# Kernel tuning notes

Measured on AMD Instinct MI355X. Metric: run time of the kernel, lower is better.

The kernel has to match this reference:

```python
import jax, jax.numpy as jnp
import numpy as np

DIM = 512
HEADS = 8
DIM_HEAD = 64
INNER = HEADS * DIM_HEAD          # 512
CPB_DIM = DIM // 2                # 256 (ContinuousPositionBias hidden dim)
FF_INNER = int(DIM * 4 * 2 / 3)   # 1365 (GEGLU inner dim)
B, C, F, H, W = 2, 512, 8, 32, 32
SCALE = DIM_HEAD ** -0.5


def setup_inputs() -> dict:
    key = jax.random.key(0)
    ks = jax.random.split(key, 24)
    def rnd(k, shape, s=0.02):
        return jax.random.normal(k, shape, jnp.float32) * s
    return {
        "x": jax.random.normal(ks[0], (B, C, F, W, W), jnp.float32)[:, :, :, :H, :],
        # spatial attention
        "sa_gamma": jnp.ones((DIM,), jnp.float32),
        "sa_wq": rnd(ks[1], (DIM, INNER)),
        "sa_wkv": rnd(ks[2], (DIM, 2 * INNER)),
        "sa_wo": rnd(ks[3], (INNER, DIM)),
        # temporal attention
        "ta_gamma": jnp.ones((DIM,), jnp.float32),
        "ta_wq": rnd(ks[4], (DIM, INNER)),
        "ta_wkv": rnd(ks[5], (DIM, 2 * INNER)),
        "ta_wo": rnd(ks[6], (INNER, DIM)),
        # spatial ContinuousPositionBias MLP (num_dims=2, layers=2)
        "sp_w1": rnd(ks[7], (2, CPB_DIM), 0.1), "sp_b1": jnp.zeros((CPB_DIM,), jnp.float32),
        "sp_w2": rnd(ks[8], (CPB_DIM, CPB_DIM), 0.05), "sp_b2": jnp.zeros((CPB_DIM,), jnp.float32),
        "sp_w3": rnd(ks[9], (CPB_DIM, HEADS), 0.05), "sp_b3": jnp.zeros((HEADS,), jnp.float32),
        # temporal ContinuousPositionBias MLP (num_dims=1)
        "tp_w1": rnd(ks[10], (1, CPB_DIM), 0.1), "tp_b1": jnp.zeros((CPB_DIM,), jnp.float32),
        "tp_w2": rnd(ks[11], (CPB_DIM, CPB_DIM), 0.05), "tp_b2": jnp.zeros((CPB_DIM,), jnp.float32),
        "tp_w3": rnd(ks[12], (CPB_DIM, HEADS), 0.05), "tp_b3": jnp.zeros((HEADS,), jnp.float32),
        # FeedForward: Conv3d 1x1 (no bias) -> GEGLU -> RMSNorm -> Conv3d 1x1
        "ff_win": rnd(ks[13], (DIM, 2 * FF_INNER)),
        "ff_gamma": jnp.ones((FF_INNER,), jnp.float32),
        "ff_wout": rnd(ks[14], (FF_INNER, DIM)),
    }


def _rms_last(x, g):
    # torch: F.normalize(x, dim=-1) * sqrt(C) * gamma
    nrm = jnp.sqrt(jnp.sum(x * x, axis=-1, keepdims=True))
    return x / jnp.maximum(nrm, 1e-12) * jnp.sqrt(jnp.float32(x.shape[-1])) * g


def _mlp_bias(rel, w1, b1, w2, b2, w3, b3):
    h = jax.nn.silu(rel @ w1 + b1)
    h = jax.nn.silu(h @ w2 + b2)
    return h @ w3 + b3  # [R, heads]


def _cpb_2d(h, w, params):
    ry = jnp.arange(-(h - 1), h, dtype=jnp.float32)
    rx = jnp.arange(-(w - 1), w, dtype=jnp.float32)
    gy, gx = jnp.meshgrid(ry, rx, indexing='ij')
    rel = jnp.stack([gy, gx], -1).reshape(-1, 2)          # [(2h-1)(2w-1), 2]
    tab = _mlp_bias(rel, *params)                          # [R, heads]
    py, px = jnp.meshgrid(jnp.arange(h), jnp.arange(w), indexing='ij')
    pos = jnp.stack([py.reshape(-1), px.reshape(-1)], -1)  # [n, 2]
    d = pos[:, None, :] - pos[None, :, :]                  # [n, n, 2]
    idx = (d[..., 0] + h - 1) * (2 * w - 1) + (d[..., 1] + w - 1)
    return jnp.transpose(tab[idx], (2, 0, 1))              # [heads, n, n]


def _cpb_1d(f, params):
    rel = jnp.arange(-(f - 1), f, dtype=jnp.float32)[:, None]
    tab = _mlp_bias(rel, *params)                          # [2f-1, heads]
    p = jnp.arange(f)
    idx = p[:, None] - p[None, :] + f - 1
    return jnp.transpose(tab[idx], (2, 0, 1))              # [heads, f, f]


def _attn(x, gamma, wq, wkv, wo, bias):
    # x: [b, n, c]; manual softmax(QK^T*scale + bias)V (flash disabled by pos_bias)
    xn = _rms_last(x, gamma)
    q = xn @ wq
    k, v = jnp.split(xn @ wkv, 2, axis=-1)
    b, n, _ = q.shape
    rs = lambda t: t.reshape(b, n, HEADS, DIM_HEAD).transpose(0, 2, 1, 3)
    q, k, v = rs(q), rs(k), rs(v)
    s = jnp.einsum('bhid,bhjd->bhij', q, k) * SCALE + bias[None]
    a = jax.nn.softmax(s, axis=-1)
    o = jnp.einsum('bhij,bhjd->bhid', a, v)
    o = o.transpose(0, 2, 1, 3).reshape(b, n, INNER)
    return o @ wo


def _ff(x, win, gamma, wout):
    # x: [b, f, h, w, c] channel-last; Conv3d 1x1 == channel einsum
    hdn = jnp.einsum('bfhwc,co->bfhwo', x, win)
    a, gate = jnp.split(hdn, 2, axis=-1)
    y = a * jax.nn.gelu(gate, approximate=False)           # GEGLU (torch exact gelu)
    # shift_token: chunk channels, shift second half by +1 frame
    c1 = (FF_INNER + 1) // 2
    t1, t2 = y[..., :c1], y[..., c1:]
    t2 = jnp.pad(t2, ((0, 0), (1, 0), (0, 0), (0, 0), (0, 0)))[:, :-1]
    y = jnp.concatenate([t1, t2], axis=-1)
    yn = _rms_last(y, gamma)                               # RMSNorm over channels
    return jnp.einsum('bfhwi,ic->bfhwc', yn, wout)


def reference(x, sa_gamma, sa_wq, sa_wkv, sa_wo, ta_gamma, ta_wq, ta_wkv, ta_wo,
              sp_w1, sp_b1, sp_w2, sp_b2, sp_w3, sp_b3,
              tp_w1, tp_b1, tp_w2, tp_b2, tp_w3, tp_b3,
              ff_win, ff_gamma, ff_wout):
    b, c, f, h, w = x.shape
    xl = jnp.transpose(x, (0, 2, 3, 4, 1))                 # b f h w c
    # spatial attention over (h w) tokens, batched over (b f)
    xs = xl.reshape(b * f, h * w, c)
    sp_bias = _cpb_2d(h, w, (sp_w1, sp_b1, sp_w2, sp_b2, sp_w3, sp_b3))
    xs = _attn(xs, sa_gamma, sa_wq, sa_wkv, sa_wo, sp_bias) + xs
    xv = xs.reshape(b, f, h, w, c)
    # temporal attention over f tokens, batched over (b h w)
    xt = jnp.transpose(xv, (0, 2, 3, 1, 4)).reshape(b * h * w, f, c)
    tp_bias = _cpb_1d(f, (tp_w1, tp_b1, tp_w2, tp_b2, tp_w3, tp_b3))
    xt = _attn(xt, ta_gamma, ta_wq, ta_wkv, ta_wo, tp_bias) + xt
    xv = jnp.transpose(xt.reshape(b, h, w, f, c), (0, 3, 1, 2, 4))
    # GEGLU feedforward with token shift
    xv = _ff(xv, ff_win, ff_gamma, ff_wout) + xv
    return jnp.transpose(xv, (0, 4, 1, 2, 3))              # b c f h w
```

## Files before the change

kernel.cpp:

```cpp
#include <hip/hip_runtime.h>
#include <cstdint>
#include <cstddef>

typedef __bf16 bf16_t;
typedef __bf16 bf16x8 __attribute__((ext_vector_type(8)));
typedef float floatx4 __attribute__((ext_vector_type(4)));

__device__ __forceinline__ float wred_sum(float v) {
#pragma unroll
  for (int off = 32; off > 0; off >>= 1) v += __shfl_xor(v, off);
  return v;
}
__device__ __forceinline__ void async16(const void* g, void* l) {
  __builtin_amdgcn_global_load_lds((const __attribute__((address_space(1))) void*)g,
                                   (__attribute__((address_space(3))) void*)l, 16, 0, 0);
}

template <bool OUT_BF16, bool RESID>
__global__ __launch_bounds__(256) void st_gemm(
    const bf16_t* __restrict__ A, const bf16_t* __restrict__ B, void* Cp,
    const float* Res, int M, int N, int K, int lda, int ldb, int ldc, int nb1,
    long long sa1, long long sa2, long long sb1, long long sb2,
    long long sc1, long long sc2) {
  __shared__ bf16_t sA[128 * 32];
  __shared__ bf16_t sB[128 * 32];
  const int z = blockIdx.z;
  const int z1 = z % nb1, z2 = z / nb1;
  A += z1 * sa1 + z2 * sa2;
  B += z1 * sb1 + z2 * sb2;
  const long long coff = z1 * sc1 + z2 * sc2;
  const int tid = threadIdx.x;
  const int bm = blockIdx.x, bn = blockIdx.y;
  const int lane = tid & 63;
  const int wave = tid >> 6;
  const int wm = (wave >> 1) * 64, wn = (wave & 1) * 64;
  const int rowf = lane & 15, kq = (lane >> 4) * 8;

  floatx4 acc[4][4];
#pragma unroll
  for (int i = 0; i < 4; ++i)
#pragma unroll
    for (int j = 0; j < 4; ++j) acc[i][j] = floatx4{0.f, 0.f, 0.f, 0.f};

  for (int kt = 0; kt < K; kt += 32) {
#pragma unroll
    for (int it = 0; it < 2; ++it) {
      int slot = it * 256 + tid;
      int mi = slot >> 2, kc = slot & 3;
      int ar = bm * 128 + mi; if (ar > M - 1) ar = M - 1;
      int br = bn * 128 + mi; if (br > N - 1) br = N - 1;
      async16(A + (size_t)ar * lda + kt + kc * 8, (char*)sA + slot * 16);
      async16(B + (size_t)br * ldb + kt + kc * 8, (char*)sB + slot * 16);
    }
    __syncthreads();
    bf16x8 af[4], bv[4];
#pragma unroll
    for (int i = 0; i < 4; ++i) {
      af[i] = *(const bf16x8*)(sA + (wm + i * 16 + rowf) * 32 + kq);
      bv[i] = *(const bf16x8*)(sB + (wn + i * 16 + rowf) * 32 + kq);
    }
#pragma unroll
    for (int i = 0; i < 4; ++i)
#pragma unroll
      for (int j = 0; j < 4; ++j)
        acc[i][j] = __builtin_amdgcn_mfma_f32_16x16x32_bf16(af[i], bv[j], acc[i][j], 0, 0, 0);
    __syncthreads();
  }

  const int colBase = bn * 128 + wn + (lane & 15);
  const int rowBase = bm * 128 + wm + (lane >> 4) * 4;
#pragma unroll
  for (int i = 0; i < 4; ++i) {
#pragma unroll
    for (int j = 0; j < 4; ++j) {
      int col = colBase + j * 16;
      if (col >= N) continue;
#pragma unroll
      for (int r = 0; r < 4; ++r) {
        int row = rowBase + i * 16 + r;
        if (row >= M) continue;
        long long idx = coff + (long long)row * ldc + col;
        float v = acc[i][j][r];
        if (RESID) v += Res[idx];
        if (OUT_BF16) ((bf16_t*)Cp)[idx] = (bf16_t)v;
        else          ((float*)Cp)[idx] = v;
      }
    }
  }
}

__global__ __launch_bounds__(256) void st_transpose2d(
    const float* __restrict__ in, float* __restrict__ out, int R, int Cc,
    long long inb, long long outb) {
  __shared__ float tile[32][33];
  const int ct = blockIdx.x, rt = blockIdx.y, b = blockIdx.z;
  in += (long long)b * inb;
  out += (long long)b * outb;
  const int tx = threadIdx.x & 31, ty = threadIdx.x >> 5;
#pragma unroll
  for (int k = 0; k < 4; ++k) {
    int r = rt * 32 + ty + k * 8;
    int c = ct * 32 + tx;
    tile[ty + k * 8][tx] = in[(size_t)r * Cc + c];
  }
  __syncthreads();
#pragma unroll
  for (int k = 0; k < 4; ++k) {
    int c = ct * 32 + ty + k * 8;
    int r = rt * 32 + tx;
    out[(size_t)c * R + r] = tile[tx][ty + k * 8];
  }
}

__global__ void st_wtrans(const float* __restrict__ src, bf16_t* __restrict__ dst,
                          int K, int Kpad, int N, int srcld, int coloff, long total) {
  long idx = (long)blockIdx.x * 256 + threadIdx.x;
  if (idx >= total) return;
  int kp = (int)(idx % Kpad);
  int n = (int)(idx / Kpad);
  float v = (kp < K) ? src[(size_t)kp * srcld + coloff + n] : 0.f;
  dst[idx] = (bf16_t)v;
}

__global__ __launch_bounds__(256) void st_cpb(
    const float* __restrict__ w1, const float* __restrict__ b1,
    const float* __restrict__ w2, const float* __restrict__ b2,
    const float* __restrict__ w3, const float* __restrict__ b3,
    bf16_t* __restrict__ tab2d, float* __restrict__ tab1d, int two_d) {
  const int pos = blockIdx.x, t = threadIdx.x;
  float r0, r1 = 0.f;
  if (two_d) { r0 = (float)(pos / 63 - 31); r1 = (float)(pos % 63 - 31); }
  else { r0 = (float)(pos - 7); }
  __shared__ float sh[256];
  float h = r0 * w1[t] + (two_d ? r1 * w1[256 + t] : 0.f) + b1[t];
  h = h / (1.f + expf(-h));
  sh[t] = h;
  __syncthreads();
  float h2 = b2[t];
  for (int j = 0; j < 256; ++j) h2 += sh[j] * w2[j * 256 + t];
  h2 = h2 / (1.f + expf(-h2));
  __syncthreads();
  sh[t] = h2;
  __syncthreads();
  if (t < 8) {
    float o = b3[t];
    for (int j = 0; j < 256; ++j) o += sh[j] * w3[j * 8 + t];
    if (two_d) tab2d[t * 4000 + pos] = (bf16_t)o;
    else tab1d[t * 15 + pos] = o;
  }
}

__global__ __launch_bounds__(256) void st_rmsnorm(const float* __restrict__ x,
                                                  const float* __restrict__ gamma,
                                                  bf16_t* __restrict__ y) {
  const int token = blockIdx.x * 4 + (threadIdx.x >> 6);
  const int lane = threadIdx.x & 63;
  const float* xr = x + (size_t)token * 512;
  float v[8];
  float ss = 0.f;
#pragma unroll
  for (int k = 0; k < 8; ++k) { v[k] = xr[k * 64 + lane]; ss += v[k] * v[k]; }
  ss = wred_sum(ss);
  const float r = 22.627416998f / fmaxf(sqrtf(ss), 1e-12f);
  bf16_t* yr = y + (size_t)token * 512;
#pragma unroll
  for (int k = 0; k < 8; ++k) yr[k * 64 + lane] = (bf16_t)(v[k] * r * gamma[k * 64 + lane]);
}

__global__ __launch_bounds__(256) void st_vtrans(const bf16_t* __restrict__ qkv,
                                                 bf16_t* __restrict__ vT) {
  __shared__ float tile[32][33];
  const int jt = blockIdx.x, dt = blockIdx.y, z = blockIdx.z;
  const int bf = z >> 3, h = z & 7;
  const int tx = threadIdx.x & 31, ty = threadIdx.x >> 5;
#pragma unroll
  for (int k = 0; k < 4; ++k) {
    int j = jt * 32 + ty + k * 8;
    int d = dt * 32 + tx;
    tile[ty + k * 8][tx] = (float)qkv[((size_t)(bf * 1024 + j)) * 1536 + 1024 + h * 64 + d];
  }
  __syncthreads();
#pragma unroll
  for (int k = 0; k < 4; ++k) {
    int d = dt * 32 + ty + k * 8;
    int j = jt * 32 + tx;
    vT[((size_t)z * 64 + d) * 1024 + j] = (bf16_t)tile[tx][ty + k * 8];
  }
}

__global__ __launch_bounds__(256, 3) void st_flash(
    const bf16_t* __restrict__ qkv, const bf16_t* __restrict__ vT,
    const bf16_t* __restrict__ tabb, bf16_t* __restrict__ ob) {
  __shared__ __align__(16) bf16_t ldsK[2][64 * 64];
  __shared__ __align__(16) bf16_t ldsV[2][64 * 64];
  __shared__ __align__(16) bf16_t ldsP[4 * 32 * 64];
  __shared__ __align__(16) bf16_t ldsT[2216];
  const int qtile = blockIdx.x;
  const int z = blockIdx.y;
  const int bf = z >> 3, h = z & 7;
  const int tid = threadIdx.x;
  const int lane = tid & 63, wave = tid >> 6;
  const int cl = lane & 15, g = lane >> 4;
  const size_t qkvBase = (size_t)bf * 1024 * 1536 + h * 64;
  const int eoff = (qtile * 252) & ~7;
  const bf16_t* Kp = qkv + qkvBase + 512;
  const bf16_t* Vp = vT + (size_t)z * 65536;

#pragma unroll
  for (int it = 0; it < 4; ++it) {
    int s = it * 256 + tid;
    int row = s >> 3, c = s & 7;
    int cs = c ^ (row & 7);
    async16(qkv + qkvBase + (size_t)(qtile * 128 + row) * 1536 + cs * 8,
            (char*)ldsP + s * 16);
  }
#pragma unroll
  for (int it = 0; it < 2; ++it) {
    int s = it * 256 + tid;
    if (s < 277) async16(tabb + h * 4000 + eoff + s * 8, (char*)ldsT + s * 16);
  }
#pragma unroll
  for (int it = 0; it < 2; ++it) {
    int s = it * 256 + tid;
    int row = s >> 3, c = s & 7;
    int cs = c ^ (row & 7);
    async16(Kp + (size_t)row * 1536 + cs * 8, (char*)ldsK[0] + s * 16);
    async16(Vp + (size_t)row * 1024 + cs * 8, (char*)ldsV[0] + s * 16);
  }
  __syncthreads();
  bf16x8 aq[2][2];
#pragma unroll
  for (int it = 0; it < 2; ++it)
#pragma unroll
    for (int ks = 0; ks < 2; ++ks) {
      int row = wave * 32 + it * 16 + cl;
      int cs = (g + ks * 4) ^ (row & 7);
      aq[it][ks] = *(const bf16x8*)(ldsP + row * 64 + cs * 8);
    }
  __syncthreads();

  int fiB[2][4];
#pragma unroll
  for (int it = 0; it < 2; ++it)
#pragma unroll
    for (int r = 0; r < 4; ++r) {
      int i = qtile * 128 + wave * 32 + it * 16 + g * 4 + r;
      fiB[it][r] = (i >> 5) * 63 + (i & 31) + 1984 - eoff;
    }
  float lsum[2][4];
  floatx4 oacc[2][4];
#pragma unroll
  for (int it = 0; it < 2; ++it)
#pragma unroll
    for (int r = 0; r < 4; ++r) lsum[it][r] = 0.f;
#pragma unroll
  for (int it = 0; it < 2; ++it)
#pragma unroll
    for (int dt = 0; dt < 4; ++dt) oacc[it][dt] = floatx4{0.f, 0.f, 0.f, 0.f};

  bf16_t* ldsPw = ldsP + wave * (32 * 64);

#pragma unroll 2
  for (int t = 0; t < 16; ++t) {
    const int p = t & 1;
    if (t < 15) {
      const int j1 = (t + 1) * 64;
#pragma unroll
      for (int it = 0; it < 2; ++it) {
        int s = it * 256 + tid;
        int row = s >> 3, c = s & 7;
        int cs = c ^ (row & 7);
        async16(Kp + (size_t)(j1 + row) * 1536 + cs * 8, (char*)ldsK[p ^ 1] + s * 16);
        async16(Vp + (size_t)row * 1024 + j1 + cs * 8, (char*)ldsV[p ^ 1] + s * 16);
      }
    }
    const int j0 = t * 64;
    floatx4 sacc[2][4];
#pragma unroll
    for (int it = 0; it < 2; ++it)
#pragma unroll
      for (int jt = 0; jt < 4; ++jt) sacc[it][jt] = floatx4{0.f, 0.f, 0.f, 0.f};
#pragma unroll
    for (int ks = 0; ks < 2; ++ks) {
#pragma unroll
      for (int jt = 0; jt < 4; ++jt) {
        int col = jt * 16 + cl;
        bf16x8 bk = *(const bf16x8*)(ldsK[p] + col * 64 + ((g + ks * 4) ^ (col & 7)) * 8);
#pragma unroll
        for (int it = 0; it < 2; ++it)
          sacc[it][jt] = __builtin_amdgcn_mfma_f32_16x16x32_bf16(aq[it][ks], bk, sacc[it][jt], 0, 0, 0);
      }
    }
#pragma unroll
    for (int jt = 0; jt < 4; ++jt) {
      int j = j0 + jt * 16 + cl;
      int fj = (j >> 5) * 63 + (j & 31);
      int pg = (jt * 2 + (cl >> 3));
#pragma unroll
      for (int it = 0; it < 2; ++it) {
#pragma unroll
        for (int r = 0; r < 4; ++r) {
          float e = __expf(sacc[it][jt][r] * 0.125f + (float)ldsT[fiB[it][r] - fj]);
          lsum[it][r] += e;
          int prow = it * 16 + g * 4 + r;
          ldsPw[prow * 64 + (pg ^ (prow & 7)) * 8 + (cl & 7)] = (bf16_t)e;
        }
      }
    }
#pragma unroll
    for (int ks = 0; ks < 2; ++ks) {
      bf16x8 ap[2];
#pragma unroll
      for (int it = 0; it < 2; ++it)
        ap[it] = *(const bf16x8*)(ldsPw + (it * 16 + cl) * 64 + ((g + ks * 4) ^ (cl & 7)) * 8);
#pragma unroll
      for (int dt = 0; dt < 4; ++dt) {
        int d = dt * 16 + cl;
        bf16x8 bv = *(const bf16x8*)(ldsV[p] + d * 64 + ((g + ks * 4) ^ (d & 7)) * 8);
#pragma unroll
        for (int it = 0; it < 2; ++it)
          oacc[it][dt] = __builtin_amdgcn_mfma_f32_16x16x32_bf16(ap[it], bv, oacc[it][dt], 0, 0, 0);
      }
    }
    __syncthreads();
  }
#pragma unroll
  for (int it = 0; it < 2; ++it)
#pragma unroll
    for (int r = 0; r < 4; ++r) {
#pragma unroll
      for (int x = 1; x < 16; x <<= 1) lsum[it][r] += __shfl_xor(lsum[it][r], x);
      lsum[it][r] = 1.f / lsum[it][r];
    }
#pragma unroll
  for (int it = 0; it < 2; ++it) {
#pragma unroll
    for (int r = 0; r < 4; ++r) {
      int i = qtile * 128 + wave * 32 + it * 16 + g * 4 + r;
      size_t base = ((size_t)bf * 1024 + i) * 512 + h * 64;
#pragma unroll
      for (int dt = 0; dt < 4; ++dt)
        ob[base + dt * 16 + cl] = (bf16_t)(oacc[it][dt][r] * lsum[it][r]);
    }
  }
}

__global__ __launch_bounds__(256) void st_tattn2(const bf16_t* __restrict__ qkv,
                                                 const float* __restrict__ tabf,
                                                 bf16_t* __restrict__ o) {
  const int wg = blockIdx.x * 4 + (threadIdx.x >> 6);
  const int bhw = wg >> 3, head = wg & 7;
  const int lane = threadIdx.x & 63;
  const size_t base = (size_t)bhw * 8 * 1536 + head * 64 + lane;
  float q[8], k[8], v[8];
#pragma unroll
  for (int f = 0; f < 8; ++f) {
    q[f] = (float)qkv[base + (size_t)f * 1536];
    k[f] = (float)qkv[base + (size_t)f * 1536 + 512];
    v[f] = (float)qkv[base + (size_t)f * 1536 + 1024];
  }
  float p[64];
#pragma unroll
  for (int i = 0; i < 8; ++i)
#pragma unroll
    for (int j = 0; j < 8; ++j) p[i * 8 + j] = q[i] * k[j];
#pragma unroll
  for (int st = 32; st >= 1; st >>= 1) {
    const bool hi = (lane & st) != 0;
#pragma unroll
    for (int m = 0; m < st; ++m) {
      float give = hi ? p[m] : p[m + st];
      float keep = hi ? p[m + st] : p[m];
      p[m] = keep + __shfl_xor(give, st);
    }
  }
  const int i = lane >> 3, j = lane & 7;
  float e = __expf(p[0] * 0.125f + tabf[head * 15 + i - j + 7]);
  float sm = e;
  sm += __shfl_xor(sm, 1);
  sm += __shfl_xor(sm, 2);
  sm += __shfl_xor(sm, 4);
  const float prob = e / sm;
  float acc[8];
#pragma unroll
  for (int ii = 0; ii < 8; ++ii) acc[ii] = 0.f;
#pragma unroll
  for (int ii = 0; ii < 8; ++ii)
#pragma unroll
    for (int jj = 0; jj < 8; ++jj)
      acc[ii] += __shfl(prob, ii * 8 + jj) * v[jj];
#pragma unroll
  for (int ii = 0; ii < 8; ++ii)
    o[(size_t)(bhw * 8 + ii) * 512 + head * 64 + lane] = (bf16_t)acc[ii];
}

__global__ void st_permute(const float* __restrict__ in, float* __restrict__ out, int dir,
                           bf16_t* __restrict__ out2) {
  size_t idx = (size_t)blockIdx.x * 256 + threadIdx.x;
  int c = (int)(idx & 511);
  size_t r = idx >> 9;
  size_t src;
  if (dir == 0) {
    int f = (int)(r & 7);
    int hw = (int)((r >> 3) & 1023);
    int b = (int)(r >> 13);
    src = ((((size_t)b * 8 + f) * 1024 + hw) << 9) + c;
  } else {
    int hw = (int)(r & 1023);
    int f = (int)((r >> 10) & 7);
    int b = (int)(r >> 13);
    src = ((((size_t)b * 1024 + hw) * 8 + f) << 9) + c;
  }
  float v = in[src];
  out[idx] = v;
  if (out2) out2[idx] = (bf16_t)v;
}

__global__ __launch_bounds__(256) void st_glu(const bf16_t* __restrict__ hdn,
                                              const float* __restrict__ gamma,
                                              bf16_t* __restrict__ yn) {
  const int t = blockIdx.x;
  const int tid = threadIdx.x;
  const int f = (t >> 10) & 7;
  float y[6];
  float ss = 0.f;
#pragma unroll
  for (int kk = 0; kk < 6; ++kk) {
    int c = kk * 256 + tid;
    float yv = 0.f;
    if (c < 1365) {
      long src = t;
      bool valid = true;
      if (c >= 683) { if (f == 0) valid = false; else src = t - 1024; }
      if (valid) {
        float av = (float)hdn[src * 2730 + c];
        float gv = (float)hdn[src * 2730 + 1365 + c];
        yv = av * 0.5f * gv * (1.f + erff(gv * 0.70710678f));
      }
    }
    y[kk] = yv;
    ss += yv * yv;
  }
  __shared__ float red[4];
  ss = wred_sum(ss);
  if ((tid & 63) == 0) red[tid >> 6] = ss;
  __syncthreads();
  ss = red[0] + red[1] + red[2] + red[3];
  const float r = sqrtf(1365.f) / fmaxf(sqrtf(ss), 1e-12f);
#pragma unroll
  for (int kk = 0; kk < 6; ++kk) {
    int c = kk * 256 + tid;
    if (c < 1365) yn[(size_t)t * 1376 + c] = (bf16_t)(y[kk] * r * gamma[c]);
  }
  if (tid < 11) yn[(size_t)t * 1376 + 1365 + tid] = (bf16_t)0.f;
}

extern "C" void kernel_launch(void* const* d_in, const int* in_sizes, int n_in,
                              void* d_out, int out_size, void* d_ws, size_t ws_size,
                              hipStream_t stream) {
  const float* x        = (const float*)d_in[0];
  const float* sa_gamma = (const float*)d_in[1];
  const float* sa_wq    = (const float*)d_in[2];
  const float* sa_wkv   = (const float*)d_in[3];
  const float* sa_wo    = (const float*)d_in[4];
  const float* ta_gamma = (const float*)d_in[5];
  const float* ta_wq    = (const float*)d_in[6];
  const float* ta_wkv   = (const float*)d_in[7];
  const float* ta_wo    = (const float*)d_in[8];
  const float* sp_w1 = (const float*)d_in[9];
  const float* sp_b1 = (const float*)d_in[10];
  const float* sp_w2 = (const float*)d_in[11];
  const float* sp_b2 = (const float*)d_in[12];
  const float* sp_w3 = (const float*)d_in[13];
  const float* sp_b3 = (const float*)d_in[14];
  const float* tp_w1 = (const float*)d_in[15];
  const float* tp_b1 = (const float*)d_in[16];
  const float* tp_w2 = (const float*)d_in[17];
  const float* tp_b2 = (const float*)d_in[18];
  const float* tp_w3 = (const float*)d_in[19];
  const float* tp_b3 = (const float*)d_in[20];
  const float* ff_win   = (const float*)d_in[21];
  const float* ff_gamma = (const float*)d_in[22];
  const float* ff_wout  = (const float*)d_in[23];
  float* outp = (float*)d_out;

  char* ws = (char*)d_ws;
  size_t off = 0;
  auto alloc = [&](size_t bytes) -> char* {
    char* p = ws + off;
    off += (bytes + 255) & ~(size_t)255;
    return p;
  };
  const long T = 16384;
  float*  xs  = (float*)alloc((size_t)T * 512 * 4);
  bf16_t* xn  = (bf16_t*)alloc((size_t)T * 512 * 2);
  char*   R2  = alloc((size_t)T * 1536 * 2);
  char*   R3  = alloc((size_t)T * 1536 * 2);
  bf16_t* ynb = (bf16_t*)alloc((size_t)T * 1376 * 2);
  bf16_t* wqkvT_sa = (bf16_t*)alloc(1536ULL * 512 * 2);
  bf16_t* woT_sa   = (bf16_t*)alloc(512ULL * 512 * 2);
  bf16_t* wqkvT_ta = (bf16_t*)alloc(1536ULL * 512 * 2);
  bf16_t* woT_ta   = (bf16_t*)alloc(512ULL * 512 * 2);
  bf16_t* winT  = (bf16_t*)alloc(2730ULL * 512 * 2);
  bf16_t* woutT = (bf16_t*)alloc(512ULL * 1376 * 2);
  bf16_t* tabb  = (bf16_t*)alloc(8 * 4000 * 2);
  float*  tabf  = (float*)alloc(8 * 15 * 4);

  bf16_t* qkv  = (bf16_t*)R2;
  bf16_t* hdn  = (bf16_t*)R2;
  bf16_t* vT   = (bf16_t*)R3;
  bf16_t* ob_s = (bf16_t*)(R3 + (size_t)T * 512 * 2);
  float*  xt   = (float*)R3;
  bf16_t* ob_t = (bf16_t*)(R3 + (size_t)T * 512 * 4);

  st_transpose2d<<<dim3(256, 16, 2), 256, 0, stream>>>(x, xs, 512, 8192,
                                                       (long long)512 * 8192, (long long)512 * 8192);
  auto wt = [&](const float* src, bf16_t* dst, int K, int Kpad, int N, int srcld, int coloff) {
    long tot = (long)N * Kpad;
    st_wtrans<<<dim3((tot + 255) / 256), 256, 0, stream>>>(src, dst, K, Kpad, N, srcld, coloff, tot);
  };
  wt(sa_wq, wqkvT_sa, 512, 512, 512, 512, 0);
  wt(sa_wkv, wqkvT_sa + 512 * 512, 512, 512, 1024, 1024, 0);
  wt(sa_wo, woT_sa, 512, 512, 512, 512, 0);
  wt(ta_wq, wqkvT_ta, 512, 512, 512, 512, 0);
  wt(ta_wkv, wqkvT_ta + 512 * 512, 512, 512, 1024, 1024, 0);
  wt(ta_wo, woT_ta, 512, 512, 512, 512, 0);
  wt(ff_win, winT, 512, 512, 2730, 2730, 0);
  wt(ff_wout, woutT, 1365, 1376, 512, 512, 0);
  st_cpb<<<dim3(3969), 256, 0, stream>>>(sp_w1, sp_b1, sp_w2, sp_b2, sp_w3, sp_b3, tabb, tabf, 1);
  st_cpb<<<dim3(15), 256, 0, stream>>>(tp_w1, tp_b1, tp_w2, tp_b2, tp_w3, tp_b3, tabb, tabf, 0);

  st_rmsnorm<<<dim3(4096), 256, 0, stream>>>(xs, sa_gamma, xn);
  st_gemm<true, false><<<dim3(128, 12, 1), 256, 0, stream>>>(
      xn, wqkvT_sa, (void*)qkv, nullptr, 16384, 1536, 512, 512, 512, 1536, 1, 0, 0, 0, 0, 0, 0);
  st_vtrans<<<dim3(32, 2, 128), 256, 0, stream>>>(qkv, vT);
  st_flash<<<dim3(8, 128), 256, 0, stream>>>(qkv, vT, tabb, ob_s);
  st_gemm<false, true><<<dim3(128, 4, 1), 256, 0, stream>>>(
      ob_s, woT_sa, (void*)xs, xs, 16384, 512, 512, 512, 512, 512, 1, 0, 0, 0, 0, 0, 0);

  st_permute<<<dim3(32768), 256, 0, stream>>>(xs, xt, 0, nullptr);
  st_rmsnorm<<<dim3(4096), 256, 0, stream>>>(xt, ta_gamma, xn);
  st_gemm<true, false><<<dim3(128, 12, 1), 256, 0, stream>>>(
      xn, wqkvT_ta, (void*)qkv, nullptr, 16384, 1536, 512, 512, 512, 1536, 1, 0, 0, 0, 0, 0, 0);
  st_tattn2<<<dim3(4096), 256, 0, stream>>>(qkv, tabf, ob_t);
  st_gemm<false, true><<<dim3(128, 4, 1), 256, 0, stream>>>(
      ob_t, woT_ta, (void*)xt, xt, 16384, 512, 512, 512, 512, 512, 1, 0, 0, 0, 0, 0, 0);
  st_permute<<<dim3(32768), 256, 0, stream>>>(xt, xs, 1, xn);

  st_gemm<true, false><<<dim3(128, 22, 1), 256, 0, stream>>>(
      xn, winT, (void*)hdn, nullptr, 16384, 2730, 512, 512, 512, 2730, 1, 0, 0, 0, 0, 0, 0);
  st_glu<<<dim3(16384), 256, 0, stream>>>(hdn, ff_gamma, ynb);
  st_gemm<false, true><<<dim3(128, 4, 1), 256, 0, stream>>>(
      ynb, woutT, (void*)xs, xs, 16384, 512, 1376, 1376, 1376, 512, 1, 0, 0, 0, 0, 0, 0);

  st_transpose2d<<<dim3(16, 256, 2), 256, 0, stream>>>(xs, outp, 8192, 512,
                                                       (long long)8192 * 512, (long long)8192 * 512);
}
```

Baseline: 743.7 us.

## Fuse permutes and GEGLU into GEMM epilogues, restructure flash softmax layout

Drops both standalone permute kernels by writing the attention output-projection results directly into permuted row order from the GEMM epilogue, with the second one also emitting a bf16 copy. Interleaves the GEGLU weight columns so the FF-in GEMM computes the gated GELU in its epilogue and writes only half-width output. The flash kernel is rewritten to compute S transposed, use exp2 with log2e folded into the scale and bias table, and do vectorized P and output stores. The goal is less global memory traffic and fewer launches, at the cost of scattered epilogue writes and more complex index maps.

```diff
diff --git a/kernel.cpp b/kernel.cpp
--- a/kernel.cpp
+++ b/kernel.cpp
@@ -4,6 +4,7 @@
 
 typedef __bf16 bf16_t;
 typedef __bf16 bf16x8 __attribute__((ext_vector_type(8)));
+typedef __bf16 bf16x4 __attribute__((ext_vector_type(4)));
 typedef float floatx4 __attribute__((ext_vector_type(4)));
 
 __device__ __forceinline__ float wred_sum(float v) {
@@ -16,9 +17,9 @@
                                    (__attribute__((address_space(3))) void*)l, 16, 0, 0);
 }
 
-template <bool OUT_BF16, bool RESID>
+template <int MODE>
 __global__ __launch_bounds__(256) void st_gemm(
-    const bf16_t* __restrict__ A, const bf16_t* __restrict__ B, void* Cp,
+    const bf16_t* __restrict__ A, const bf16_t* __restrict__ B, void* Cp, void* Cp2,
     const float* Res, int M, int N, int K, int lda, int ldb, int ldc, int nb1,
     long long sa1, long long sa2, long long sb1, long long sb2,
     long long sc1, long long sc2) {
@@ -67,8 +68,31 @@
     __syncthreads();
   }
 
-  const int colBase = bn * 128 + wn + (lane & 15);
+  const int cl = lane & 15;
   const int rowBase = bm * 128 + wm + (lane >> 4) * 4;
+  if (MODE == 5) {
+    bf16_t* yb = (bf16_t*)Cp;
+    const int cg0 = ((bn * 128 + wn) >> 5) * 16;
+#pragma unroll
+    for (int i = 0; i < 4; ++i) {
+#pragma unroll
+      for (int p = 0; p < 2; ++p) {
+        int c = cg0 + p * 16 + cl;
+        if (c >= 1365) continue;
+#pragma unroll
+        for (int r = 0; r < 4; ++r) {
+          int row = rowBase + i * 16 + r;
+          if (row >= M) continue;
+          float a = acc[i][2 * p][r];
+          float gt = acc[i][2 * p + 1][r];
+          float y = a * 0.5f * gt * (1.f + erff(gt * 0.70710678f));
+          yb[(size_t)row * ldc + c] = (bf16_t)y;
+        }
+      }
+    }
+    return;
+  }
+  const int colBase = bn * 128 + wn + cl;
 #pragma unroll
   for (int i = 0; i < 4; ++i) {
 #pragma unroll
@@ -79,11 +103,21 @@
       for (int r = 0; r < 4; ++r) {
         int row = rowBase + i * 16 + r;
         if (row >= M) continue;
-        long long idx = coff + (long long)row * ldc + col;
+        long long inidx = coff + (long long)row * ldc + col;
         float v = acc[i][j][r];
-        if (RESID) v += Res[idx];
-        if (OUT_BF16) ((bf16_t*)Cp)[idx] = (bf16_t)v;
-        else          ((float*)Cp)[idx] = v;
+        if (MODE >= 2) v += Res[inidx];
+        if (MODE == 0) { ((float*)Cp)[inidx] = v; }
+        else if (MODE == 1) { ((bf16_t*)Cp)[inidx] = (bf16_t)v; }
+        else if (MODE == 2) { ((float*)Cp)[inidx] = v; }
+        else if (MODE == 3) {
+          int orow = (row & ~8191) | ((row & 1023) << 3) | ((row >> 10) & 7);
+          ((float*)Cp)[coff + (long long)orow * ldc + col] = v;
+        } else if (MODE == 4) {
+          int orow = (row & ~8191) | ((row & 7) << 10) | ((row >> 3) & 1023);
+          long long oidx = coff + (long long)orow * ldc + col;
+          ((float*)Cp)[oidx] = v;
+          ((bf16_t*)Cp2)[oidx] = (bf16_t)v;
+        }
       }
     }
   }
@@ -119,6 +153,21 @@
   int kp = (int)(idx % Kpad);
   int n = (int)(idx / Kpad);
   float v = (kp < K) ? src[(size_t)kp * srcld + coloff + n] : 0.f;
+  dst[idx] = (bf16_t)v;
+}
+
+__global__ void st_wtrans_geglu(const float* __restrict__ src, bf16_t* __restrict__ dst,
+                                long total) {
+  long idx = (long)blockIdx.x * 256 + threadIdx.x;
+  if (idx >= total) return;
+  int kp = (int)(idx & 511);
+  int n = (int)(idx >> 9);
+  int c = ((n >> 5) << 4) + (n & 15);
+  float v = 0.f;
+  if (c < 1365) {
+    int srccol = c + (((n >> 4) & 1) ? 1365 : 0);
+    v = src[(size_t)kp * 2730 + srccol];
+  }
   dst[idx] = (bf16_t)v;
 }
 
@@ -145,7 +194,7 @@
   if (t < 8) {
     float o = b3[t];
     for (int j = 0; j < 256; ++j) o += sh[j] * w3[j * 8 + t];
-    if (two_d) tab2d[t * 4000 + pos] = (bf16_t)o;
+    if (two_d) tab2d[t * 4000 + pos] = (bf16_t)(o * 1.4426950408889634f);
     else tab1d[t * 15 + pos] = o;
   }
 }
@@ -239,26 +288,21 @@
     }
   __syncthreads();
 
-  int fiB[2][4];
-#pragma unroll
-  for (int it = 0; it < 2; ++it)
-#pragma unroll
-    for (int r = 0; r < 4; ++r) {
-      int i = qtile * 128 + wave * 32 + it * 16 + g * 4 + r;
-      fiB[it][r] = (i >> 5) * 63 + (i & 31) + 1984 - eoff;
-    }
-  float lsum[2][4];
-  floatx4 oacc[2][4];
-#pragma unroll
-  for (int it = 0; it < 2; ++it)
-#pragma unroll
-    for (int r = 0; r < 4; ++r) lsum[it][r] = 0.f;
-#pragma unroll
-  for (int it = 0; it < 2; ++it)
-#pragma unroll
-    for (int dt = 0; dt < 4; ++dt) oacc[it][dt] = floatx4{0.f, 0.f, 0.f, 0.f};
+  int fiB[2];
+#pragma unroll
+  for (int it = 0; it < 2; ++it) {
+    int i = qtile * 128 + wave * 32 + it * 16 + cl;
+    fiB[it] = (i >> 5) * 63 + (i & 31) + 1984 - eoff;
+  }
+  float lsum[2] = {0.f, 0.f};
+  floatx4 oacc[4][2];
+#pragma unroll
+  for (int dt = 0; dt < 4; ++dt)
+#pragma unroll
+    for (int it = 0; it < 2; ++it) oacc[dt][it] = floatx4{0.f, 0.f, 0.f, 0.f};
 
   bf16_t* ldsPw = ldsP + wave * (32 * 64);
+  const float SC = 0.18033688011112042f;
 
 #pragma unroll 2
   for (int t = 0; t < 16; ++t) {
@@ -275,72 +319,75 @@
       }
     }
     const int j0 = t * 64;
-    floatx4 sacc[2][4];
-#pragma unroll
-    for (int it = 0; it < 2; ++it)
-#pragma unroll
-      for (int jt = 0; jt < 4; ++jt) sacc[it][jt] = floatx4{0.f, 0.f, 0.f, 0.f};
+    floatx4 sacc[4][2];
+#pragma unroll
+    for (int jt = 0; jt < 4; ++jt)
+#pragma unroll
+      for (int it = 0; it < 2; ++it) sacc[jt][it] = floatx4{0.f, 0.f, 0.f, 0.f};
 #pragma unroll
     for (int ks = 0; ks < 2; ++ks) {
 #pragma unroll
       for (int jt = 0; jt < 4; ++jt) {
-        int col = jt * 16 + cl;
-        bf16x8 bk = *(const bf16x8*)(ldsK[p] + col * 64 + ((g + ks * 4) ^ (col & 7)) * 8);
+        int row = jt * 16 + cl;
+        bf16x8 kf = *(const bf16x8*)(ldsK[p] + row * 64 + (((ks * 4 + g) ^ (row & 7))) * 8);
 #pragma unroll
         for (int it = 0; it < 2; ++it)
-          sacc[it][jt] = __builtin_amdgcn_mfma_f32_16x16x32_bf16(aq[it][ks], bk, sacc[it][jt], 0, 0, 0);
+          sacc[jt][it] = __builtin_amdgcn_mfma_f32_16x16x32_bf16(kf, aq[it][ks], sacc[jt][it], 0, 0, 0);
       }
     }
 #pragma unroll
     for (int jt = 0; jt < 4; ++jt) {
-      int j = j0 + jt * 16 + cl;
-      int fj = (j >> 5) * 63 + (j & 31);
-      int pg = (jt * 2 + (cl >> 3));
+      int jb = j0 + jt * 16 + g * 4;
+      int fjb = (jb >> 5) * 63 + (jb & 31);
+      int gg = jt * 2 + (g >> 1);
 #pragma unroll
       for (int it = 0; it < 2; ++it) {
-#pragma unroll
-        for (int r = 0; r < 4; ++r) {
-          float e = __expf(sacc[it][jt][r] * 0.125f + (float)ldsT[fiB[it][r] - fj]);
-          lsum[it][r] += e;
-          int prow = it * 16 + g * 4 + r;
-          ldsPw[prow * 64 + (pg ^ (prow & 7)) * 8 + (cl & 7)] = (bf16_t)e;
-        }
+        int idx0 = fiB[it] - fjb;
+        float e0 = __builtin_exp2f(sacc[jt][it][0] * SC + (float)ldsT[idx0]);
+        float e1 = __builtin_exp2f(sacc[jt][it][1] * SC + (float)ldsT[idx0 - 1]);
+        float e2 = __builtin_exp2f(sacc[jt][it][2] * SC + (float)ldsT[idx0 - 2]);
+        float e3 = __builtin_exp2f(sacc[jt][it][3] * SC + (float)ldsT[idx0 - 3]);
+        lsum[it] += (e0 + e1) + (e2 + e3);
+        bf16x4 pv = {(bf16_t)e0, (bf16_t)e1, (bf16_t)e2, (bf16_t)e3};
+        int prow = it * 16 + cl;
+        *(bf16x4*)((char*)ldsPw + prow * 128 + ((gg ^ (cl & 7)) * 16 + (g & 1) * 8)) = pv;
       }
     }
 #pragma unroll
     for (int ks = 0; ks < 2; ++ks) {
-      bf16x8 ap[2];
+      bf16x8 pB[2];
 #pragma unroll
       for (int it = 0; it < 2; ++it)
-        ap[it] = *(const bf16x8*)(ldsPw + (it * 16 + cl) * 64 + ((g + ks * 4) ^ (cl & 7)) * 8);
+        pB[it] = *(const bf16x8*)((char*)ldsPw + (it * 16 + cl) * 128 +
+                                  (((ks * 4 + g) ^ (cl & 7)) * 16));
 #pragma unroll
       for (int dt = 0; dt < 4; ++dt) {
-        int d = dt * 16 + cl;
-        bf16x8 bv = *(const bf16x8*)(ldsV[p] + d * 64 + ((g + ks * 4) ^ (d & 7)) * 8);
+        int row = dt * 16 + cl;
+        bf16x8 vf = *(const bf16x8*)(ldsV[p] + row * 64 + (((ks * 4 + g) ^ (row & 7))) * 8);
 #pragma unroll
         for (int it = 0; it < 2; ++it)
-          oacc[it][dt] = __builtin_amdgcn_mfma_f32_16x16x32_bf16(ap[it], bv, oacc[it][dt], 0, 0, 0);
+          oacc[dt][it] = __builtin_amdgcn_mfma_f32_16x16x32_bf16(vf, pB[it], oacc[dt][it], 0, 0, 0);
       }
     }
     __syncthreads();
   }
-#pragma unroll
-  for (int it = 0; it < 2; ++it)
-#pragma unroll
-    for (int r = 0; r < 4; ++r) {
-#pragma unroll
-      for (int x = 1; x < 16; x <<= 1) lsum[it][r] += __shfl_xor(lsum[it][r], x);
-      lsum[it][r] = 1.f / lsum[it][r];
-    }
+  float inv[2];
 #pragma unroll
   for (int it = 0; it < 2; ++it) {
-#pragma unroll
-    for (int r = 0; r < 4; ++r) {
-      int i = qtile * 128 + wave * 32 + it * 16 + g * 4 + r;
-      size_t base = ((size_t)bf * 1024 + i) * 512 + h * 64;
-#pragma unroll
-      for (int dt = 0; dt < 4; ++dt)
-        ob[base + dt * 16 + cl] = (bf16_t)(oacc[it][dt][r] * lsum[it][r]);
+    float s = lsum[it];
+    s += __shfl_xor(s, 16);
+    s += __shfl_xor(s, 32);
+    inv[it] = 1.f / s;
+  }
+#pragma unroll
+  for (int it = 0; it < 2; ++it) {
+    int i = qtile * 128 + wave * 32 + it * 16 + cl;
+    size_t base = ((size_t)bf * 1024 + i) * 512 + h * 64 + g * 4;
+#pragma unroll
+    for (int dt = 0; dt < 4; ++dt) {
+      bf16x4 ov = {(bf16_t)(oacc[dt][it][0] * inv[it]), (bf16_t)(oacc[dt][it][1] * inv[it]),
+                   (bf16_t)(oacc[dt][it][2] * inv[it]), (bf16_t)(oacc[dt][it][3] * inv[it])};
+      *(bf16x4*)(ob + base + dt * 16) = ov;
     }
   }
 }
@@ -394,52 +441,26 @@
     o[(size_t)(bhw * 8 + ii) * 512 + head * 64 + lane] = (bf16_t)acc[ii];
 }
 
-__global__ void st_permute(const float* __restrict__ in, float* __restrict__ out, int dir,
-                           bf16_t* __restrict__ out2) {
-  size_t idx = (size_t)blockIdx.x * 256 + threadIdx.x;
-  int c = (int)(idx & 511);
-  size_t r = idx >> 9;
-  size_t src;
-  if (dir == 0) {
-    int f = (int)(r & 7);
-    int hw = (int)((r >> 3) & 1023);
-    int b = (int)(r >> 13);
-    src = ((((size_t)b * 8 + f) * 1024 + hw) << 9) + c;
-  } else {
-    int hw = (int)(r & 1023);
-    int f = (int)((r >> 10) & 7);
-    int b = (int)(r >> 13);
-    src = ((((size_t)b * 1024 + hw) * 8 + f) << 9) + c;
-  }
-  float v = in[src];
-  out[idx] = v;
-  if (out2) out2[idx] = (bf16_t)v;
-}
-
-__global__ __launch_bounds__(256) void st_glu(const bf16_t* __restrict__ hdn,
+__global__ __launch_bounds__(256) void st_glu(const bf16_t* __restrict__ y,
                                               const float* __restrict__ gamma,
                                               bf16_t* __restrict__ yn) {
   const int t = blockIdx.x;
   const int tid = threadIdx.x;
   const int f = (t >> 10) & 7;
-  float y[6];
+  float yv[6];
   float ss = 0.f;
 #pragma unroll
   for (int kk = 0; kk < 6; ++kk) {
     int c = kk * 256 + tid;
-    float yv = 0.f;
+    float v = 0.f;
     if (c < 1365) {
       long src = t;
       bool valid = true;
       if (c >= 683) { if (f == 0) valid = false; else src = t - 1024; }
-      if (valid) {
-        float av = (float)hdn[src * 2730 + c];
-        float gv = (float)hdn[src * 2730 + 1365 + c];
-        yv = av * 0.5f * gv * (1.f + erff(gv * 0.70710678f));
-      }
-    }
-    y[kk] = yv;
-    ss += yv * yv;
+      if (valid) v = (float)y[src * 1365 + c];
+    }
+    yv[kk] = v;
+    ss += v * v;
   }
   __shared__ float red[4];
   ss = wred_sum(ss);
@@ -450,7 +471,7 @@
 #pragma unroll
   for (int kk = 0; kk < 6; ++kk) {
     int c = kk * 256 + tid;
-    if (c < 1365) yn[(size_t)t * 1376 + c] = (bf16_t)(y[kk] * r * gamma[c]);
+    if (c < 1365) yn[(size_t)t * 1376 + c] = (bf16_t)(yv[kk] * r * gamma[c]);
   }
   if (tid < 11) yn[(size_t)t * 1376 + 1365 + tid] = (bf16_t)0.f;
 }
@@ -496,22 +517,23 @@
   bf16_t* xn  = (bf16_t*)alloc((size_t)T * 512 * 2);
   char*   R2  = alloc((size_t)T * 1536 * 2);
   char*   R3  = alloc((size_t)T * 1536 * 2);
-  bf16_t* ynb = (bf16_t*)alloc((size_t)T * 1376 * 2);
+  char*   R4  = alloc((size_t)T * 1376 * 2);
   bf16_t* wqkvT_sa = (bf16_t*)alloc(1536ULL * 512 * 2);
   bf16_t* woT_sa   = (bf16_t*)alloc(512ULL * 512 * 2);
   bf16_t* wqkvT_ta = (bf16_t*)alloc(1536ULL * 512 * 2);
   bf16_t* woT_ta   = (bf16_t*)alloc(512ULL * 512 * 2);
-  bf16_t* winT  = (bf16_t*)alloc(2730ULL * 512 * 2);
+  bf16_t* winT  = (bf16_t*)alloc(2752ULL * 512 * 2);
   bf16_t* woutT = (bf16_t*)alloc(512ULL * 1376 * 2);
   bf16_t* tabb  = (bf16_t*)alloc(8 * 4000 * 2);
   float*  tabf  = (float*)alloc(8 * 15 * 4);
 
   bf16_t* qkv  = (bf16_t*)R2;
-  bf16_t* hdn  = (bf16_t*)R2;
+  bf16_t* ybuf = (bf16_t*)R2;
   bf16_t* vT   = (bf16_t*)R3;
-  bf16_t* ob_s = (bf16_t*)(R3 + (size_t)T * 512 * 2);
   float*  xt   = (float*)R3;
-  bf16_t* ob_t = (bf16_t*)(R3 + (size_t)T * 512 * 4);
+  bf16_t* ob_s = xn;
+  bf16_t* ob_t = (bf16_t*)R4;
+  bf16_t* ynb  = (bf16_t*)R4;
 
   st_transpose2d<<<dim3(256, 16, 2), 256, 0, stream>>>(x, xs, 512, 8192,
                                                        (long long)512 * 8192, (long long)512 * 8192);
@@ -525,33 +547,31 @@
   wt(ta_wq, wqkvT_ta, 512, 512, 512, 512, 0);
   wt(ta_wkv, wqkvT_ta + 512 * 512, 512, 512, 1024, 1024, 0);
   wt(ta_wo, woT_ta, 512, 512, 512, 512, 0);
-  wt(ff_win, winT, 512, 512, 2730, 2730, 0);
+  st_wtrans_geglu<<<dim3((2752 * 512) / 256), 256, 0, stream>>>(ff_win, winT, 2752L * 512);
   wt(ff_wout, woutT, 1365, 1376, 512, 512, 0);
   st_cpb<<<dim3(3969), 256, 0, stream>>>(sp_w1, sp_b1, sp_w2, sp_b2, sp_w3, sp_b3, tabb, tabf, 1);
   st_cpb<<<dim3(15), 256, 0, stream>>>(tp_w1, tp_b1, tp_w2, tp_b2, tp_w3, tp_b3, tabb, tabf, 0);
 
   st_rmsnorm<<<dim3(4096), 256, 0, stream>>>(xs, sa_gamma, xn);
-  st_gemm<true, false><<<dim3(128, 12, 1), 256, 0, stream>>>(
-      xn, wqkvT_sa, (void*)qkv, nullptr, 16384, 1536, 512, 512, 512, 1536, 1, 0, 0, 0, 0, 0, 0);
+  st_gemm<1><<<dim3(128, 12, 1), 256, 0, stream>>>(
+      xn, wqkvT_sa, (void*)qkv, nullptr, nullptr, 16384, 1536, 512, 512, 512, 1536, 1, 0, 0, 0, 0, 0, 0);
   st_vtrans<<<dim3(32, 2, 128), 256, 0, stream>>>(qkv, vT);
   st_flash<<<dim3(8, 128), 256, 0, stream>>>(qkv, vT, tabb, ob_s);
-  st_gemm<false, true><<<dim3(128, 4, 1), 256, 0, stream>>>(
-      ob_s, woT_sa, (void*)xs, xs, 16384, 512, 512, 512, 512, 512, 1, 0, 0, 0, 0, 0, 0);
-
-  st_permute<<<dim3(32768), 256, 0, stream>>>(xs, xt, 0, nullptr);
+  st_gemm<3><<<dim3(128, 4, 1), 256, 0, stream>>>(
+      ob_s, woT_sa, (void*)xt, nullptr, xs, 16384, 512, 512, 512, 512, 512, 1, 0, 0, 0, 0, 0, 0);
+
   st_rmsnorm<<<dim3(4096), 256, 0, stream>>>(xt, ta_gamma, xn);
-  st_gemm<true, false><<<dim3(128, 12, 1), 256, 0, stream>>>(
-      xn, wqkvT_ta, (void*)qkv, nullptr, 16384, 1536, 512, 512, 512, 1536, 1, 0, 0, 0, 0, 0, 0);
+  st_gemm<1><<<dim3(128, 12, 1), 256, 0, stream>>>(
+      xn, wqkvT_ta, (void*)qkv, nullptr, nullptr, 16384, 1536, 512, 512, 512, 1536, 1, 0, 0, 0, 0, 0, 0);
   st_tattn2<<<dim3(4096), 256, 0, stream>>>(qkv, tabf, ob_t);
-  st_gemm<false, true><<<dim3(128, 4, 1), 256, 0, stream>>>(
-      ob_t, woT_ta, (void*)xt, xt, 16384, 512, 512, 512, 512, 512, 1, 0, 0, 0, 0, 0, 0);
-  st_permute<<<dim3(32768), 256, 0, stream>>>(xt, xs, 1, xn);
-
-  st_gemm<true, false><<<dim3(128, 22, 1), 256, 0, stream>>>(
-      xn, winT, (void*)hdn, nullptr, 16384, 2730, 512, 512, 512, 2730, 1, 0, 0, 0, 0, 0, 0);
-  st_glu<<<dim3(16384), 256, 0, stream>>>(hdn, ff_gamma, ynb);
-  st_gemm<false, true><<<dim3(128, 4, 1), 256, 0, stream>>>(
-      ynb, woutT, (void*)xs, xs, 16384, 512, 1376, 1376, 1376, 512, 1, 0, 0, 0, 0, 0, 0);
+  st_gemm<4><<<dim3(128, 4, 1), 256, 0, stream>>>(
+      ob_t, woT_ta, (void*)xs, (void*)xn, xt, 16384, 512, 512, 512, 512, 512, 1, 0, 0, 0, 0, 0, 0);
+
+  st_gemm<5><<<dim3(128, 22, 1), 256, 0, stream>>>(
+      xn, winT, (void*)ybuf, nullptr, nullptr, 16384, 2752, 512, 512, 512, 1365, 1, 0, 0, 0, 0, 0, 0);
+  st_glu<<<dim3(16384), 256, 0, stream>>>(ybuf, ff_gamma, ynb);
+  st_gemm<2><<<dim3(128, 4, 1), 256, 0, stream>>>(
+      ynb, woutT, (void*)xs, nullptr, xs, 16384, 512, 1376, 1376, 1376, 512, 1, 0, 0, 0, 0, 0, 0);
 
   st_transpose2d<<<dim3(16, 256, 2), 256, 0, stream>>>(xs, outp, 8192, 512,
                                                        (long long)8192 * 512, (long long)8192 * 512);
```

New measurement: 704.5 us. 5.3% less time.
